# Kernel tuning notes

Hardware: AMD Instinct MI355X
Metric: run time of the kernel (lower is better)

Reference implementation:

```python
import jax, jax.numpy as jnp
import numpy as np

NF = 64   # num_feat
DG = 8    # deformable_groups (also conv groups)
B, H, W = 4, 96, 96
K = 9     # 3x3 kernel positions


def _conv(x, w, b, padding=1, dilation=1, groups=1):
    out = jax.lax.conv_general_dilated(
        x, w, (1, 1), [(padding, padding), (padding, padding)],
        rhs_dilation=(dilation, dilation),
        dimension_numbers=('NCHW', 'OIHW', 'NCHW'),
        feature_group_count=groups)
    return out + b[None, :, None, None]


def _lrelu(t):
    return jnp.where(t >= 0, t, 0.1 * t)


def _cat_align(a, b):
    # channel-interleaved concat: [a0,b0,a1,b1,...]
    Bn, k, h, w = a.shape
    return jnp.stack([a, b], axis=2).reshape(Bn, 2 * k, h, w)


def _deform_conv(x, offset, mask, weight, bias, dilation, padding):
    # DCNv2 modulated deformable conv, stride 1.
    Bn, C, h, w = x.shape
    Cpg = C // DG
    off = offset.reshape(Bn, DG, K, 2, h, w)          # (dy, dx) per group/kernel pos
    m = mask.reshape(Bn, DG, K, h, w)
    ky = (jnp.repeat(jnp.arange(3), 3) * dilation - padding).astype(x.dtype)  # (K,)
    kx = (jnp.tile(jnp.arange(3), 3) * dilation - padding).astype(x.dtype)
    hs = jnp.arange(h, dtype=x.dtype)
    ws = jnp.arange(w, dtype=x.dtype)
    py = off[:, :, :, 0] + ky[None, None, :, None, None] + hs[None, None, None, :, None]
    px = off[:, :, :, 1] + kx[None, None, :, None, None] + ws[None, None, None, None, :]
    y0f = jnp.floor(py); x0f = jnp.floor(px)
    ly = (py - y0f)[:, :, None]  # broadcast over Cpg
    lx = (px - x0f)[:, :, None]
    y0 = y0f.astype(jnp.int32); x0 = x0f.astype(jnp.int32)
    xg = x.reshape(Bn, DG, Cpg, h * w)

    def gather(yi, xi):
        inb = ((yi >= 0) & (yi < h) & (xi >= 0) & (xi < w))
        idx = (jnp.clip(yi, 0, h - 1) * w + jnp.clip(xi, 0, w - 1)).reshape(Bn, DG, 1, K * h * w)
        v = jnp.take_along_axis(xg, jnp.broadcast_to(idx, (Bn, DG, Cpg, K * h * w)), axis=3)
        return v.reshape(Bn, DG, Cpg, K, h, w) * inb[:, :, None].astype(x.dtype)

    v00 = gather(y0, x0); v01 = gather(y0, x0 + 1)
    v10 = gather(y0 + 1, x0); v11 = gather(y0 + 1, x0 + 1)
    val = (v00 * (1 - ly) * (1 - lx) + v01 * (1 - ly) * lx
           + v10 * ly * (1 - lx) + v11 * ly * lx) * m[:, :, None]
    sampled = val.reshape(Bn, C, K, h, w)
    out = jnp.einsum('bckhw,ock->bohw', sampled, weight.reshape(weight.shape[0], C, K))
    return out + bias[None, :, None, None]


def _dcn(x, off_feat, om_w, om_b, w, b, dilation):
    pad = dilation  # int(3/2)*dilation
    out = _conv(off_feat, om_w, om_b, padding=pad, dilation=dilation)
    o1, o2, msk = jnp.split(out, 3, axis=1)
    offset = jnp.concatenate([o1, o2], axis=1)
    mask = jax.nn.sigmoid(msk)
    return _deform_conv(x, offset, mask, w, b, dilation, pad)


def setup_inputs() -> dict:
    key = jax.random.key(0)
    ks = iter(jax.random.split(key, 64))
    def rn(shape, s=0.05):
        return jax.random.normal(next(ks), shape, jnp.float32) * s
    d = {}
    d['nbr_feat'] = jax.random.normal(next(ks), (B, NF, H, W), jnp.float32)
    d['ref_feat'] = jax.random.normal(next(ks), (B, NF, H, W), jnp.float32)
    for lv, has3 in [('l3', False), ('l2', True), ('l1', True)]:
        d[f'oc1_w_{lv}'] = rn((NF, 2 * NF // DG, 3, 3)); d[f'oc1_b_{lv}'] = rn((NF,))
        oc2_in = 2 * NF if has3 else NF
        d[f'oc2_w_{lv}'] = rn((NF, oc2_in // DG, 3, 3)); d[f'oc2_b_{lv}'] = rn((NF,))
        if has3:
            d[f'oc3_w_{lv}'] = rn((NF, NF // DG, 3, 3)); d[f'oc3_b_{lv}'] = rn((NF,))
            d[f'fc_w_{lv}'] = rn((NF, 2 * NF // DG, 3, 3)); d[f'fc_b_{lv}'] = rn((NF,))
        d[f'om_w_{lv}'] = rn((DG * 3 * K, NF, 3, 3), 0.01); d[f'om_b_{lv}'] = rn((DG * 3 * K,), 0.01)
        d[f'dcn_w_{lv}'] = rn((NF, NF, 3, 3)); d[f'dcn_b_{lv}'] = rn((NF,))
    d['cas_oc1_w'] = rn((NF, 2 * NF // DG, 3, 3)); d['cas_oc1_b'] = rn((NF,))
    d['cas_oc2_w'] = rn((NF, NF // DG, 3, 3)); d['cas_oc2_b'] = rn((NF,))
    d['cas_om_w'] = rn((DG * 3 * K, NF, 3, 3), 0.01); d['cas_om_b'] = rn((DG * 3 * K,), 0.01)
    d['cas_w'] = rn((NF, NF, 3, 3)); d['cas_b'] = rn((NF,))
    return d


def reference(nbr_feat, ref_feat,
              oc1_w_l3, oc1_b_l3, oc2_w_l3, oc2_b_l3, om_w_l3, om_b_l3, dcn_w_l3, dcn_b_l3,
              oc1_w_l2, oc1_b_l2, oc2_w_l2, oc2_b_l2, oc3_w_l2, oc3_b_l2, fc_w_l2, fc_b_l2,
              om_w_l2, om_b_l2, dcn_w_l2, dcn_b_l2,
              oc1_w_l1, oc1_b_l1, oc2_w_l1, oc2_b_l1, oc3_w_l1, oc3_b_l1, fc_w_l1, fc_b_l1,
              om_w_l1, om_b_l1, dcn_w_l1, dcn_b_l1,
              cas_oc1_w, cas_oc1_b, cas_oc2_w, cas_oc2_b, cas_om_w, cas_om_b, cas_w, cas_b):
    # level 3 (dilation 5)
    off = _lrelu(_conv(_cat_align(nbr_feat, ref_feat), oc1_w_l3, oc1_b_l3, groups=DG))
    off = _lrelu(_conv(off, oc2_w_l3, oc2_b_l3, groups=DG))
    feat = _lrelu(_dcn(nbr_feat, off, om_w_l3, om_b_l3, dcn_w_l3, dcn_b_l3, 5))
    to, tf = off, feat
    # level 2 (dilation 3)
    off = _lrelu(_conv(_cat_align(nbr_feat, ref_feat), oc1_w_l2, oc1_b_l2, groups=DG))
    off = _lrelu(_conv(_cat_align(off, to), oc2_w_l2, oc2_b_l2, groups=DG))
    off = _lrelu(_conv(off, oc3_w_l2, oc3_b_l2, groups=DG))
    feat = _dcn(nbr_feat, off, om_w_l2, om_b_l2, dcn_w_l2, dcn_b_l2, 3)
    feat = _lrelu(_conv(_cat_align(feat, tf), fc_w_l2, fc_b_l2, groups=DG))
    to, tf = off, feat
    # level 1 (dilation 1), no lrelu on feat
    off = _lrelu(_conv(_cat_align(nbr_feat, ref_feat), oc1_w_l1, oc1_b_l1, groups=DG))
    off = _lrelu(_conv(_cat_align(off, to), oc2_w_l1, oc2_b_l1, groups=DG))
    off = _lrelu(_conv(off, oc3_w_l1, oc3_b_l1, groups=DG))
    feat = _dcn(nbr_feat, off, om_w_l1, om_b_l1, dcn_w_l1, dcn_b_l1, 1)
    feat = _conv(_cat_align(feat, tf), fc_w_l1, fc_b_l1, groups=DG)
    # cascade
    off = _cat_align(feat, ref_feat)
    off = _lrelu(_conv(_lrelu(_conv(off, cas_oc1_w, cas_oc1_b, groups=DG)), cas_oc2_w, cas_oc2_b, groups=DG))
    feat = _lrelu(_dcn(feat, off, cas_om_w, cas_om_b, cas_w, cas_b, 1))
    return feat
```

## Files before the change

### kernel.cpp

```cpp
#include <hip/hip_runtime.h>

#define BATCH 4
#define NFEAT 64
#define DGRP 8
#define HH 96
#define WW 96
#define HWP (HH*WW)

typedef short short4a __attribute__((ext_vector_type(4)));
typedef short short8 __attribute__((ext_vector_type(8)));
typedef float f32x4 __attribute__((ext_vector_type(4)));
typedef float f32x16 __attribute__((ext_vector_type(16)));

__device__ inline short f2bf(float f) {
  union { float f; unsigned u; } v; v.f = f;
  unsigned r = v.u + 0x7fff + ((v.u >> 16) & 1);
  return (short)(r >> 16);
}
__device__ inline float bf2f(short s) {
  return __uint_as_float(((unsigned)(unsigned short)s) << 16);
}

__device__ __forceinline__ void barrier_keep_vmcnt() {
  asm volatile("s_waitcnt lgkmcnt(0)" ::: "memory");
  __builtin_amdgcn_s_barrier();
  asm volatile("" ::: "memory");
}

__global__ __launch_bounds__(256) void prep_om(
    const float* __restrict__ s0, const float* __restrict__ s1,
    const float* __restrict__ s2, const float* __restrict__ s3,
    short* __restrict__ dst) {
  int gid = blockIdx.x * 256 + threadIdx.x;
  if (gid >= 4 * 147456) return;
  int t = gid / 147456, r = gid % 147456;
  int tile = r / 18432, r2 = r % 18432;
  int kk = r2 / 512, r3 = r2 % 512;
  int lane = r3 / 8, j = r3 % 8;
  int col = lane & 31, half = lane >> 5;
  int oc = tile * 32 + col;
  int k = kk * 16 + half * 8 + j;
  int p = k >> 6, c = k & 63;
  const float* s = (t == 0) ? s0 : (t == 1) ? s1 : (t == 2) ? s2 : s3;
  float v = (oc < 216) ? s[(size_t)oc * 576 + c * 9 + p] : 0.f;
  dst[gid] = f2bf(v);
}

__global__ __launch_bounds__(256) void prep_dcnw(
    const float* __restrict__ s0, const float* __restrict__ s1,
    const float* __restrict__ s2, const float* __restrict__ s3,
    short* __restrict__ dst) {
  int gid = blockIdx.x * 256 + threadIdx.x;
  if (gid >= 4 * 36864) return;
  int t = gid / 36864, r = gid % 36864;
  int tile = r / 18432, r2 = r % 18432;
  int kk = r2 / 512, r3 = r2 % 512;
  int lane = r3 / 8, j = r3 % 8;
  int col = lane & 31, half = lane >> 5;
  int oc = tile * 32 + col;
  int k = kk * 16 + half * 8 + j;
  int p = k >> 6, c = k & 63;
  const float* s = (t == 0) ? s0 : (t == 1) ? s1 : (t == 2) ? s2 : s3;
  dst[gid] = f2bf(s[(size_t)oc * 576 + c * 9 + p]);
}

struct GwArgs {
  const float* src[12];
  int cat[12];
  int base[13];
};

__global__ __launch_bounds__(256) void prep_gw(GwArgs a, short* __restrict__ dst) {
  int gid = blockIdx.x * 256 + threadIdx.x;
  if (gid >= a.base[12]) return;
  int t = 0;
  while (gid >= a.base[t + 1]) ++t;
  int r = gid - a.base[t];
  const float* s = a.src[t];
  const int tsz = a.cat[t] ? 4608 : 2560;
  int tile = r / tsz, r2 = r % tsz;
  int kk = r2 / 512, r3 = r2 % 512;
  int lane = r3 >> 3, j = r3 & 7;
  int m = lane & 15, quad = lane >> 4;
  int oc = tile * 16 + m;
  int j32 = quad * 8 + j;
  float val = 0.f;
  if (a.cat[t]) {
    int gsel = j32 >> 4, ssel = (j32 >> 3) & 1, ch8 = j32 & 7;
    if (gsel == (m >> 3)) val = s[oc * 144 + (2 * ch8 + ssel) * 9 + kk];
  } else {
    int tapsel = j32 >> 4, gsel = (j32 >> 3) & 1, ch8 = j32 & 7;
    int p = 2 * kk + tapsel;
    if (p < 9 && gsel == (m >> 3)) val = s[oc * 72 + ch8 * 9 + p];
  }
  dst[gid] = f2bf(val);
}

__global__ __launch_bounds__(256) void transpose_bf16(
    const float* __restrict__ in0, short* __restrict__ out0,
    const float* __restrict__ in1, short* __restrict__ out1) {
  const float* in = blockIdx.z ? in1 : in0;
  short* out = blockIdx.z ? out1 : out0;
  __shared__ float s[64][65];
  const int p0 = blockIdx.x * 64;
  const int b = blockIdx.y;
  const int tx = threadIdx.x, ty = threadIdx.y;
  for (int c = ty; c < 64; c += 4)
    s[c][tx] = in[((size_t)b * NFEAT + c) * HWP + p0 + tx];
  __syncthreads();
  for (int p = ty; p < 64; p += 4)
    out[((size_t)b * HWP + p0 + p) * NFEAT + tx] = f2bf(s[tx][p]);
}

template <bool CAT, bool LRELU>
__device__ __forceinline__ void gconv_body(
    const short* __restrict__ in0, const short* __restrict__ in1,
    const short* __restrict__ Wsh, const float* __restrict__ bias,
    short* __restrict__ out, int pixbase, int b, int lid) {
  const int lane = lid & 63, t = lid >> 6;
  const int n = lane & 15, quad = lane >> 4;
  constexpr int NKK = CAT ? 9 : 5;

  short8 A[NKK];
#pragma unroll
  for (int kk = 0; kk < NKK; ++kk)
    A[kk] = *(const short8*)(Wsh + ((size_t)(t * NKK + kk) * 64 + lane) * 8);

  const short* sb;
  if (CAT) {
    sb = ((quad & 1) ? in1 : in0) + (size_t)b * HWP * 64 + (2 * t + (quad >> 1)) * 8;
  } else {
    sb = in0 + (size_t)b * HWP * 64 + (2 * t + (quad & 1)) * 8;
  }

  f32x4 acc[2] = {};
#pragma unroll
  for (int nt = 0; nt < 2; ++nt) {
    const int pix = pixbase + nt * 16 + n;
    const int yp = pix / WW, xp = pix % WW;
#pragma unroll
    for (int kk = 0; kk < NKK; ++kk) {
      const int p = CAT ? kk : (2 * kk + (quad >> 1));
      short8 B = {0, 0, 0, 0, 0, 0, 0, 0};
      if (p < 9) {
        const int sy = yp + p / 3 - 1, sx = xp + p % 3 - 1;
        if (((unsigned)sy < (unsigned)HH) && ((unsigned)sx < (unsigned)WW))
          B = *(const short8*)(sb + (size_t)(sy * WW + sx) * 64);
      }
      acc[nt] = __builtin_amdgcn_mfma_f32_16x16x32_bf16(A[kk], B, acc[nt], 0, 0, 0);
    }
  }

  const int ocb = t * 16 + quad * 4;
  const float b0 = bias[ocb], b1 = bias[ocb + 1], b2 = bias[ocb + 2], b3 = bias[ocb + 3];
#pragma unroll
  for (int nt = 0; nt < 2; ++nt) {
    float v0 = acc[nt][0] + b0, v1 = acc[nt][1] + b1;
    float v2 = acc[nt][2] + b2, v3 = acc[nt][3] + b3;
    if (LRELU) {
      v0 = (v0 >= 0.f) ? v0 : 0.1f * v0;
      v1 = (v1 >= 0.f) ? v1 : 0.1f * v1;
      v2 = (v2 >= 0.f) ? v2 : 0.1f * v2;
      v3 = (v3 >= 0.f) ? v3 : 0.1f * v3;
    }
    short4a pk = {f2bf(v0), f2bf(v1), f2bf(v2), f2bf(v3)};
    *(short4a*)(out + ((size_t)b * HWP + pixbase + nt * 16 + n) * 64 + ocb) = pk;
  }
}

template <bool CAT, bool LRELU>
__global__ __launch_bounds__(256) void gconv_mfma(
    const short* __restrict__ in0, const short* __restrict__ in1,
    const short* __restrict__ Wsh, const float* __restrict__ bias,
    short* __restrict__ out) {
  gconv_body<CAT, LRELU>(in0, in1, Wsh, bias, out, blockIdx.x * 32, blockIdx.y,
                         threadIdx.x);
}

struct Oc1Args {
  const short* W[3];
  const float* bias[3];
  short* out[3];
};

__global__ __launch_bounds__(256) void gconv_oc1x3(
    const short* __restrict__ in0, const short* __restrict__ in1, Oc1Args a) {
  const int job = blockIdx.z;
  gconv_body<true, true>(in0, in1, a.W[job], a.bias[job], a.out[job],
                         blockIdx.x * 32, blockIdx.y, threadIdx.x);
}

#define BPITCH 324
template <int D>
__device__ __forceinline__ void omconv_body(
    short* Bs,
    const short* __restrict__ pixT, const short* __restrict__ Wsh,
    const float* __restrict__ bias, short* __restrict__ out,
    int xblk, int b, int lid) {
  const int lane = lid & 63;
  const int w = lid >> 6;
  const int col = lane & 31, half = lane >> 5;
  const int pixbase = xblk * 64;

  const short* aP0 = Wsh + ((size_t)(w * 36) * 64) * 8 + (size_t)lane * 8;
  const short* aP1 = Wsh + ((size_t)((w + 4) * 36) * 64) * 8 + (size_t)lane * 8;
  const short* pixb = pixT + (size_t)b * HWP * 64;

  f32x16 acc00 = {}, acc01 = {}, acc10 = {}, acc11 = {};

  for (int i = lid; i < 64 * 5 * 8; i += 256) {
    int row = i / 40, q = i % 40;
    int p = q >> 3, c8 = q & 7;
    int pix = pixbase + row;
    int yp = pix / WW, xp = pix % WW;
    int sy = yp + (p / 3 - 1) * D, sx = xp + (p % 3 - 1) * D;
    short4a lo = {0, 0, 0, 0}, hi = {0, 0, 0, 0};
    if (((unsigned)sy < (unsigned)HH) && ((unsigned)sx < (unsigned)WW)) {
      const short* src = pixb + (size_t)(sy * WW + sx) * 64 + c8 * 8;
      lo = *(const short4a*)src;
      hi = *(const short4a*)(src + 4);
    }
    short* dst = Bs + row * BPITCH + q * 8;
    *(short4a*)dst = lo;
    *(short4a*)(dst + 4) = hi;
  }

  short4a p1lo[8], p1hi[8];
  int p1dst[8];
#pragma unroll
  for (int idx = 0; idx < 8; ++idx) {
    int i = lid + idx * 256;
    int row = i / 32, q = i % 32;
    int p = 5 + (q >> 3), c8 = q & 7;
    int pix = pixbase + row;
    int yp = pix / WW, xp = pix % WW;
    int sy = yp + (p / 3 - 1) * D, sx = xp + (p % 3 - 1) * D;
    short4a lo = {0, 0, 0, 0}, hi = {0, 0, 0, 0};
    if (((unsigned)sy < (unsigned)HH) && ((unsigned)sx < (unsigned)WW)) {
      const short* src = pixb + (size_t)(sy * WW + sx) * 64 + c8 * 8;
      lo = *(const short4a*)src;
      hi = *(const short4a*)(src + 4);
    }
    p1lo[idx] = lo;
    p1hi[idx] = hi;
    p1dst[idx] = row * BPITCH + q * 8;
  }
  barrier_keep_vmcnt();

#pragma unroll 4
  for (int kk = 0; kk < 20; ++kk) {
    short8 A0 = *(const short8*)(aP0 + (size_t)kk * 512);
    short8 A1 = *(const short8*)(aP1 + (size_t)kk * 512);
    const short* b0 = Bs + col * BPITCH + kk * 16 + half * 8;
    const short* b1 = Bs + (32 + col) * BPITCH + kk * 16 + half * 8;
    short4a l0 = *(const short4a*)b0, h0 = *(const short4a*)(b0 + 4);
    short4a l1 = *(const short4a*)b1, h1 = *(const short4a*)(b1 + 4);
    short8 B0 = {l0[0], l0[1], l0[2], l0[3], h0[0], h0[1], h0[2], h0[3]};
    short8 B1 = {l1[0], l1[1], l1[2], l1[3], h1[0], h1[1], h1[2], h1[3]};
    acc00 = __builtin_amdgcn_mfma_f32_32x32x16_bf16(A0, B0, acc00, 0, 0, 0);
    acc01 = __builtin_amdgcn_mfma_f32_32x32x16_bf16(A0, B1, acc01, 0, 0, 0);
    acc10 = __builtin_amdgcn_mfma_f32_32x32x16_bf16(A1, B0, acc10, 0, 0, 0);
    acc11 = __builtin_amdgcn_mfma_f32_32x32x16_bf16(A1, B1, acc11, 0, 0, 0);
  }
  barrier_keep_vmcnt();

#pragma unroll
  for (int idx = 0; idx < 8; ++idx) {
    short* dst = Bs + p1dst[idx];
    *(short4a*)dst = p1lo[idx];
    *(short4a*)(dst + 4) = p1hi[idx];
  }
  barrier_keep_vmcnt();

#pragma unroll 4
  for (int kk = 0; kk < 16; ++kk) {
    const int kkg = 20 + kk;
    short8 A0 = *(const short8*)(aP0 + (size_t)kkg * 512);
    short8 A1 = *(const short8*)(aP1 + (size_t)kkg * 512);
    const short* b0 = Bs + col * BPITCH + kk * 16 + half * 8;
    const short* b1 = Bs + (32 + col) * BPITCH + kk * 16 + half * 8;
    short4a l0 = *(const short4a*)b0, h0 = *(const short4a*)(b0 + 4);
    short4a l1 = *(const short4a*)b1, h1 = *(const short4a*)(b1 + 4);
    short8 B0 = {l0[0], l0[1], l0[2], l0[3], h0[0], h0[1], h0[2], h0[3]};
    short8 B1 = {l1[0], l1[1], l1[2], l1[3], h1[0], h1[1], h1[2], h1[3]};
    acc00 = __builtin_amdgcn_mfma_f32_32x32x16_bf16(A0, B0, acc00, 0, 0, 0);
    acc01 = __builtin_amdgcn_mfma_f32_32x32x16_bf16(A0, B1, acc01, 0, 0, 0);
    acc10 = __builtin_amdgcn_mfma_f32_32x32x16_bf16(A1, B0, acc10, 0, 0, 0);
    acc11 = __builtin_amdgcn_mfma_f32_32x32x16_bf16(A1, B1, acc11, 0, 0, 0);
  }

  const int pix0 = pixbase + col, pix1 = pixbase + 32 + col;
#pragma unroll
  for (int r = 0; r < 16; ++r) {
    const int rrow = (r & 3) + 8 * (r >> 2) + 4 * half;
    const int oc0 = w * 32 + rrow;
    const int oc1 = (w + 4) * 32 + rrow;
    const float bs0 = bias[oc0];
    out[((size_t)b * 216 + oc0) * HWP + pix0] = f2bf(acc00[r] + bs0);
    out[((size_t)b * 216 + oc0) * HWP + pix1] = f2bf(acc01[r] + bs0);
    if (oc1 < 216) {
      const float bs1 = bias[oc1];
      out[((size_t)b * 216 + oc1) * HWP + pix0] = f2bf(acc10[r] + bs1);
      out[((size_t)b * 216 + oc1) * HWP + pix1] = f2bf(acc11[r] + bs1);
    }
  }
}

template <int D>
__global__ __launch_bounds__(256) void omconv_mfma(
    const short* __restrict__ pixT, const short* __restrict__ Wsh,
    const float* __restrict__ bias, short* __restrict__ out) {
  __shared__ short Bs[64 * BPITCH];
  omconv_body<D>(Bs, pixT, Wsh, bias, out, blockIdx.x, blockIdx.y, threadIdx.x);
}

template <int D, bool LRELU, bool PMOUT>
__device__ __forceinline__ void dcn_body(
    char* smem,
    const short* __restrict__ xT, const short* __restrict__ om,
    const short* __restrict__ Wd, const float* __restrict__ bias,
    void* __restrict__ outv, int pb, int b, int lid) {
  short* Ls = (short*)smem;
  float* red = (float*)(smem + 36864);
  const int tx = lid & 31, ty = lid >> 5;

  {
    const int px = tx, dg = ty;
    const int pix = pb * 32 + px;
    const int yp = pix / WW, xp = pix % WW;
    const size_t bOM = (size_t)b * 216 * HWP;
    const short* xb = xT + (size_t)b * HWP * 64 + dg * 8;
    short* Sp = Ls + (size_t)((dg & 1) * 32 + px) * 8;

#pragma unroll
    for (int k = 0; k < 9; ++k) {
      float dy = bf2f(om[bOM + (size_t)(dg * 18 + 2 * k) * HWP + pix]);
      float dxv = bf2f(om[bOM + (size_t)(dg * 18 + 2 * k + 1) * HWP + pix]);
      float mr = bf2f(om[bOM + (size_t)(144 + dg * 9 + k) * HWP + pix]);
      float m = 1.f / (1.f + __expf(-mr));
      float py = (float)(yp + (k / 3 - 1) * D) + dy;
      float px_ = (float)(xp + (k % 3 - 1) * D) + dxv;
      float y0f = floorf(py), x0f = floorf(px_);
      float ly = py - y0f, lx = px_ - x0f;
      int y0 = (int)y0f, x0 = (int)x0f;
      int y1 = y0 + 1, x1 = x0 + 1;
      bool vy0 = (unsigned)y0 < (unsigned)HH, vy1 = (unsigned)y1 < (unsigned)HH;
      bool vx0 = (unsigned)x0 < (unsigned)WW, vx1 = (unsigned)x1 < (unsigned)WW;
      int cy0 = min(max(y0, 0), HH - 1), cy1 = min(max(y1, 0), HH - 1);
      int cx0 = min(max(x0, 0), WW - 1), cx1 = min(max(x1, 0), WW - 1);
      float w00 = (vy0 && vx0) ? (1.f - ly) * (1.f - lx) * m : 0.f;
      float w01 = (vy0 && vx1) ? (1.f - ly) * lx * m : 0.f;
      float w10 = (vy1 && vx0) ? ly * (1.f - lx) * m : 0.f;
      float w11 = (vy1 && vx1) ? ly * lx * m : 0.f;
      short8 s00 = *(const short8*)(xb + (size_t)(cy0 * WW + cx0) * 64);
      short8 s01 = *(const short8*)(xb + (size_t)(cy0 * WW + cx1) * 64);
      short8 s10 = *(const short8*)(xb + (size_t)(cy1 * WW + cx0) * 64);
      short8 s11 = *(const short8*)(xb + (size_t)(cy1 * WW + cx1) * 64);
      short8 pk;
#pragma unroll
      for (int cl = 0; cl < 8; ++cl) {
        float v = w00 * bf2f(s00[cl]) + w01 * bf2f(s01[cl]) +
                  w10 * bf2f(s10[cl]) + w11 * bf2f(s11[cl]);
        pk[cl] = f2bf(v);
      }
      const int kk = k * 4 + (dg >> 1);
      *(short8*)(Sp + (size_t)kk * 512) = pk;
    }
  }
  __syncthreads();

  const int lane = lid & 63, w = lid >> 6;
  const int col = lane & 31, half = lane >> 5;
  const int octile = w & 1, kh = w >> 1;
  const int pix = pb * 32 + col;

  const short* aP = Wd + ((size_t)(octile * 36) * 64 + lane) * 8;
  const short* bP = Ls + (size_t)lane * 8;

  f32x16 acc = {};
#pragma unroll 6
  for (int kk = 0; kk < 18; ++kk) {
    const int kkg = kh * 18 + kk;
    short8 A = *(const short8*)(aP + (size_t)kkg * 512);
    short8 B = *(const short8*)(bP + (size_t)kkg * 512);
    acc = __builtin_amdgcn_mfma_f32_32x32x16_bf16(A, B, acc, 0, 0, 0);
  }

  if (kh == 1) {
#pragma unroll
    for (int r = 0; r < 16; ++r) red[((size_t)octile * 64 + lane) * 17 + r] = acc[r];
  }
  __syncthreads();
  if (kh == 0) {
    const float* rp = red + ((size_t)octile * 64 + lane) * 17;
    if (PMOUT) {
      short* out = (short*)outv;
#pragma unroll
      for (int rg = 0; rg < 4; ++rg) {
        short4a pk;
#pragma unroll
        for (int i = 0; i < 4; ++i) {
          const int r = rg * 4 + i;
          const int oc = octile * 32 + i + 8 * rg + 4 * half;
          float v = acc[r] + rp[r] + bias[oc];
          if (LRELU) v = (v >= 0.f) ? v : 0.1f * v;
          pk[i] = f2bf(v);
        }
        *(short4a*)(out + ((size_t)b * HWP + pix) * 64 + octile * 32 + 8 * rg + 4 * half) = pk;
      }
    } else {
      float* out = (float*)outv;
#pragma unroll
      for (int r = 0; r < 16; ++r) {
        const int oc = octile * 32 + (r & 3) + 8 * (r >> 2) + 4 * half;
        float v = acc[r] + rp[r] + bias[oc];
        if (LRELU) v = (v >= 0.f) ? v : 0.1f * v;
        out[((size_t)b * NFEAT + oc) * HWP + pix] = v;
      }
    }
  }
}

template <int D, bool LRELU, bool PMOUT>
__global__ __launch_bounds__(256) void dcn_fused(
    const short* __restrict__ xT, const short* __restrict__ om,
    const short* __restrict__ Wd, const float* __restrict__ bias,
    void* __restrict__ outv) {
  __shared__ char smem[45568];
  dcn_body<D, LRELU, PMOUT>(smem, xT, om, Wd, bias, outv,
                            blockIdx.x, blockIdx.y, threadIdx.x);
}

template <int D>
__global__ __launch_bounds__(256) void om_gc(
    const short* __restrict__ pixT, const short* __restrict__ Wom,
    const float* __restrict__ obias, short* __restrict__ omOut,
    const short* __restrict__ g0, const short* __restrict__ g1,
    const short* __restrict__ gW, const float* __restrict__ gb,
    short* __restrict__ gout) {
  __shared__ short Bs[64 * BPITCH];
  if (blockIdx.x < 144)
    omconv_body<D>(Bs, pixT, Wom, obias, omOut, blockIdx.x, blockIdx.y, threadIdx.x);
  else
    gconv_body<true, true>(g0, g1, gW, gb, gout, (blockIdx.x - 144) * 32,
                           blockIdx.y, threadIdx.x);
}

template <int D, bool DLRELU>
__global__ __launch_bounds__(256) void dcn_gc(
    const short* __restrict__ xT, const short* __restrict__ om,
    const short* __restrict__ Wd, const float* __restrict__ dbias,
    short* __restrict__ dout,
    const short* __restrict__ g0, const short* __restrict__ gW,
    const float* __restrict__ gb, short* __restrict__ gout) {
  __shared__ char smem[45568];
  if (blockIdx.x < 288)
    dcn_body<D, DLRELU, true>(smem, xT, om, Wd, dbias, dout,
                              blockIdx.x, blockIdx.y, threadIdx.x);
  else
    gconv_body<false, true>(g0, nullptr, gW, gb, gout, (blockIdx.x - 288) * 32,
                            blockIdx.y, threadIdx.x);
}

extern "C" void kernel_launch(void* const* d_in, const int* in_sizes, int n_in,
                              void* d_out, int out_size, void* d_ws, size_t ws_size,
                              hipStream_t stream) {
  const float* nbr = (const float*)d_in[0];
  const float* ref = (const float*)d_in[1];
  auto f = [&](int i) { return (const float*)d_in[i]; };

  short* s0 = (short*)d_ws;
  const size_t PM = (size_t)BATCH * HWP * 64;
  short* omB = s0;
  short* refT = omB + 7962624;
  short* pmA = refT + PM;
  short* pmB = pmA + PM;
  short* pmC = pmB + PM;
  short* pmD = pmC + PM;
  short* pmE = pmD + PM;
  short* pmF = pmE + PM;
  short* pmG = pmF + PM;
  short* wbf = pmG + PM;
  short* wdcn = wbf + 589824;
  short* wgc = wdcn + 147456;
  short* nbrT = (short*)d_out;

  prep_om<<<(4 * 147456 + 255) / 256, 256, 0, stream>>>(f(6), f(18), f(30), f(38), wbf);
  prep_dcnw<<<(4 * 36864 + 255) / 256, 256, 0, stream>>>(f(8), f(20), f(32), f(40), wdcn);

  static const int gSrc[12] = {2, 4, 10, 12, 14, 16, 22, 24, 26, 28, 34, 36};
  static const int gCat[12] = {1, 0, 1, 1, 0, 1, 1, 1, 0, 1, 1, 0};
  GwArgs ga;
  int gb = 0;
  const short* wg[12];
  for (int t = 0; t < 12; ++t) {
    ga.src[t] = f(gSrc[t]);
    ga.cat[t] = gCat[t];
    ga.base[t] = gb;
    wg[t] = wgc + gb;
    gb += gCat[t] ? 18432 : 10240;
  }
  ga.base[12] = gb;
  prep_gw<<<(gb + 255) / 256, 256, 0, stream>>>(ga, wgc);

  short* wbf_l3 = wbf;
  short* wbf_l2 = wbf + 147456;
  short* wbf_l1 = wbf + 2 * 147456;
  short* wbf_cas = wbf + 3 * 147456;
  short* wd_l3 = wdcn;
  short* wd_l2 = wdcn + 36864;
  short* wd_l1 = wdcn + 2 * 36864;
  short* wd_cas = wdcn + 3 * 36864;

  dim3 gcGrid(288, BATCH);
  dim3 oc1Grid(288, BATCH, 3);
  dim3 omgcGrid(432, BATCH);
  dim3 dcngcGrid(576, BATCH);
  dim3 omGrid(144, BATCH);
  dim3 dfGrid(288, BATCH);
  dim3 trGrid(HWP / 64, BATCH, 2), trBlk(64, 4);

  transpose_bf16<<<trGrid, trBlk, 0, stream>>>(nbr, nbrT, ref, refT);

  Oc1Args oa;
  oa.W[0] = wg[0]; oa.bias[0] = f(3);  oa.out[0] = pmA;
  oa.W[1] = wg[2]; oa.bias[1] = f(11); oa.out[1] = pmF;
  oa.W[2] = wg[6]; oa.bias[2] = f(23); oa.out[2] = pmG;
  gconv_oc1x3<<<oc1Grid, 256, 0, stream>>>(nbrT, refT, oa);

  gconv_mfma<false, true><<<gcGrid, 256, 0, stream>>>(pmA, nullptr, wg[1], f(5), pmB);

  om_gc<5><<<omgcGrid, 256, 0, stream>>>(pmB, wbf_l3, f(7), omB,
                                         pmF, pmB, wg[3], f(13), pmD);
  dcn_gc<5, true><<<dcngcGrid, 256, 0, stream>>>(nbrT, omB, wd_l3, f(9), pmC,
                                                 pmD, wg[4], f(15), pmE);
  om_gc<3><<<omgcGrid, 256, 0, stream>>>(pmE, wbf_l2, f(19), omB,
                                         pmG, pmE, wg[7], f(25), pmB);
  dcn_gc<3, false><<<dcngcGrid, 256, 0, stream>>>(nbrT, omB, wd_l2, f(21), pmD,
                                                  pmB, wg[8], f(27), pmF);
  om_gc<1><<<omgcGrid, 256, 0, stream>>>(pmF, wbf_l1, f(31), omB,
                                         pmD, pmC, wg[5], f(17), pmA);
  dcn_fused<1, false, true><<<dfGrid, 256, 0, stream>>>(nbrT, omB, wd_l1, f(33), pmE);
  gconv_mfma<true, false><<<gcGrid, 256, 0, stream>>>(pmE, pmA, wg[9], f(29), pmB);

  gconv_mfma<true, true><<<gcGrid, 256, 0, stream>>>(pmB, refT, wg[10], f(35), pmC);
  gconv_mfma<false, true><<<gcGrid, 256, 0, stream>>>(pmC, nullptr, wg[11], f(37), pmD);
  omconv_mfma<1><<<omGrid, 256, 0, stream>>>(pmD, wbf_cas, f(39), omB);
  dcn_fused<1, true, false><<<dfGrid, 256, 0, stream>>>(pmB, omB, wd_cas, f(41), (float*)d_out);
}
```

Measured before the change: 505.3 us.

## Fuse prep kernels, halve omconv pixel tile, and alias DCN reduction smem

Merges the four preprocessing launches (input transposes plus three weight-reformat kernels) into a single fused kernel to cut launch overhead and serialization. Halves the omconv tile from 64 to 32 pixels per block, which doubles its grid and halves its LDS footprint and accumulator registers. The DCN reduction buffer now aliases the sample tile, with an added barrier, shrinking shared memory. Together these aim for higher occupancy and better SM fill, at the cost of reloading weights for each smaller tile.

```diff
diff --git a/kernel.cpp b/kernel.cpp
--- a/kernel.cpp
+++ b/kernel.cpp
@@ -27,12 +27,14 @@
   asm volatile("" ::: "memory");
 }
 
-__global__ __launch_bounds__(256) void prep_om(
-    const float* __restrict__ s0, const float* __restrict__ s1,
-    const float* __restrict__ s2, const float* __restrict__ s3,
-    short* __restrict__ dst) {
-  int gid = blockIdx.x * 256 + threadIdx.x;
-  if (gid >= 4 * 147456) return;
+struct GwArgs {
+  const float* src[12];
+  int cat[12];
+  int base[13];
+};
+
+__device__ __forceinline__ void prep_om_elem(
+    int gid, const float* const* s4, short* __restrict__ dst) {
   int t = gid / 147456, r = gid % 147456;
   int tile = r / 18432, r2 = r % 18432;
   int kk = r2 / 512, r3 = r2 % 512;
@@ -41,17 +43,12 @@
   int oc = tile * 32 + col;
   int k = kk * 16 + half * 8 + j;
   int p = k >> 6, c = k & 63;
-  const float* s = (t == 0) ? s0 : (t == 1) ? s1 : (t == 2) ? s2 : s3;
-  float v = (oc < 216) ? s[(size_t)oc * 576 + c * 9 + p] : 0.f;
+  float v = (oc < 216) ? s4[t][(size_t)oc * 576 + c * 9 + p] : 0.f;
   dst[gid] = f2bf(v);
 }
 
-__global__ __launch_bounds__(256) void prep_dcnw(
-    const float* __restrict__ s0, const float* __restrict__ s1,
-    const float* __restrict__ s2, const float* __restrict__ s3,
-    short* __restrict__ dst) {
-  int gid = blockIdx.x * 256 + threadIdx.x;
-  if (gid >= 4 * 36864) return;
+__device__ __forceinline__ void prep_dcnw_elem(
+    int gid, const float* const* s4, short* __restrict__ dst) {
   int t = gid / 36864, r = gid % 36864;
   int tile = r / 18432, r2 = r % 18432;
   int kk = r2 / 512, r3 = r2 % 512;
@@ -60,19 +57,11 @@
   int oc = tile * 32 + col;
   int k = kk * 16 + half * 8 + j;
   int p = k >> 6, c = k & 63;
-  const float* s = (t == 0) ? s0 : (t == 1) ? s1 : (t == 2) ? s2 : s3;
-  dst[gid] = f2bf(s[(size_t)oc * 576 + c * 9 + p]);
-}
-
-struct GwArgs {
-  const float* src[12];
-  int cat[12];
-  int base[13];
-};
-
-__global__ __launch_bounds__(256) void prep_gw(GwArgs a, short* __restrict__ dst) {
-  int gid = blockIdx.x * 256 + threadIdx.x;
-  if (gid >= a.base[12]) return;
+  dst[gid] = f2bf(s4[t][(size_t)oc * 576 + c * 9 + p]);
+}
+
+__device__ __forceinline__ void prep_gw_elem(
+    int gid, const GwArgs& a, short* __restrict__ dst) {
   int t = 0;
   while (gid >= a.base[t + 1]) ++t;
   int r = gid - a.base[t];
@@ -96,20 +85,35 @@
   dst[gid] = f2bf(val);
 }
 
-__global__ __launch_bounds__(256) void transpose_bf16(
-    const float* __restrict__ in0, short* __restrict__ out0,
-    const float* __restrict__ in1, short* __restrict__ out1) {
-  const float* in = blockIdx.z ? in1 : in0;
-  short* out = blockIdx.z ? out1 : out0;
+struct PrepArgs {
+  const float* nbr; const float* ref;
+  short* nbrT; short* refT;
+  const float* omS[4]; short* wbf;
+  const float* dwS[4]; short* wdcn;
+  GwArgs gw; short* wgc;
+};
+
+__global__ __launch_bounds__(256) void prep_fused(PrepArgs a) {
   __shared__ float s[64][65];
-  const int p0 = blockIdx.x * 64;
-  const int b = blockIdx.y;
-  const int tx = threadIdx.x, ty = threadIdx.y;
-  for (int c = ty; c < 64; c += 4)
-    s[c][tx] = in[((size_t)b * NFEAT + c) * HWP + p0 + tx];
-  __syncthreads();
-  for (int p = ty; p < 64; p += 4)
-    out[((size_t)b * HWP + p0 + p) * NFEAT + tx] = f2bf(s[tx][p]);
+  const int bx = blockIdx.x;
+  const int lid = threadIdx.x;
+  if (bx < 1152) {
+    const int x = bx % 144, b = (bx / 144) & 3, z = bx / 576;
+    const float* in = z ? a.ref : a.nbr;
+    short* out = z ? a.refT : a.nbrT;
+    const int p0 = x * 64;
+    const int tx = lid & 63, ty = lid >> 6;
+    for (int c = ty; c < 64; c += 4)
+      s[c][tx] = in[((size_t)b * NFEAT + c) * HWP + p0 + tx];
+    __syncthreads();
+    for (int p = ty; p < 64; p += 4)
+      out[((size_t)b * HWP + p0 + p) * NFEAT + tx] = f2bf(s[tx][p]);
+  } else {
+    const int gid = (bx - 1152) * 256 + lid;
+    if (gid < 589824) prep_om_elem(gid, a.omS, a.wbf);
+    else if (gid < 737280) prep_dcnw_elem(gid - 589824, a.dwS, a.wdcn);
+    else if (gid < 925696) prep_gw_elem(gid - 737280, a.gw, a.wgc);
+  }
 }
 
 template <bool CAT, bool LRELU>
@@ -200,15 +204,15 @@
   const int lane = lid & 63;
   const int w = lid >> 6;
   const int col = lane & 31, half = lane >> 5;
-  const int pixbase = xblk * 64;
+  const int pixbase = xblk * 32;
 
   const short* aP0 = Wsh + ((size_t)(w * 36) * 64) * 8 + (size_t)lane * 8;
   const short* aP1 = Wsh + ((size_t)((w + 4) * 36) * 64) * 8 + (size_t)lane * 8;
   const short* pixb = pixT + (size_t)b * HWP * 64;
 
-  f32x16 acc00 = {}, acc01 = {}, acc10 = {}, acc11 = {};
-
-  for (int i = lid; i < 64 * 5 * 8; i += 256) {
+  f32x16 acc00 = {}, acc10 = {};
+
+  for (int i = lid; i < 32 * 5 * 8; i += 256) {
     int row = i / 40, q = i % 40;
     int p = q >> 3, c8 = q & 7;
     int pix = pixbase + row;
@@ -225,10 +229,10 @@
     *(short4a*)(dst + 4) = hi;
   }
 
-  short4a p1lo[8], p1hi[8];
-  int p1dst[8];
-#pragma unroll
-  for (int idx = 0; idx < 8; ++idx) {
+  short4a p1lo[4], p1hi[4];
+  int p1dst[4];
+#pragma unroll
+  for (int idx = 0; idx < 4; ++idx) {
     int i = lid + idx * 256;
     int row = i / 32, q = i % 32;
     int p = 5 + (q >> 3), c8 = q & 7;
@@ -252,20 +256,15 @@
     short8 A0 = *(const short8*)(aP0 + (size_t)kk * 512);
     short8 A1 = *(const short8*)(aP1 + (size_t)kk * 512);
     const short* b0 = Bs + col * BPITCH + kk * 16 + half * 8;
-    const short* b1 = Bs + (32 + col) * BPITCH + kk * 16 + half * 8;
     short4a l0 = *(const short4a*)b0, h0 = *(const short4a*)(b0 + 4);
-    short4a l1 = *(const short4a*)b1, h1 = *(const short4a*)(b1 + 4);
     short8 B0 = {l0[0], l0[1], l0[2], l0[3], h0[0], h0[1], h0[2], h0[3]};
-    short8 B1 = {l1[0], l1[1], l1[2], l1[3], h1[0], h1[1], h1[2], h1[3]};
     acc00 = __builtin_amdgcn_mfma_f32_32x32x16_bf16(A0, B0, acc00, 0, 0, 0);
-    acc01 = __builtin_amdgcn_mfma_f32_32x32x16_bf16(A0, B1, acc01, 0, 0, 0);
     acc10 = __builtin_amdgcn_mfma_f32_32x32x16_bf16(A1, B0, acc10, 0, 0, 0);
-    acc11 = __builtin_amdgcn_mfma_f32_32x32x16_bf16(A1, B1, acc11, 0, 0, 0);
   }
   barrier_keep_vmcnt();
 
 #pragma unroll
-  for (int idx = 0; idx < 8; ++idx) {
+  for (int idx = 0; idx < 4; ++idx) {
     short* dst = Bs + p1dst[idx];
     *(short4a*)dst = p1lo[idx];
     *(short4a*)(dst + 4) = p1hi[idx];
@@ -278,31 +277,21 @@
     short8 A0 = *(const short8*)(aP0 + (size_t)kkg * 512);
     short8 A1 = *(const short8*)(aP1 + (size_t)kkg * 512);
     const short* b0 = Bs + col * BPITCH + kk * 16 + half * 8;
-    const short* b1 = Bs + (32 + col) * BPITCH + kk * 16 + half * 8;
     short4a l0 = *(const short4a*)b0, h0 = *(const short4a*)(b0 + 4);
-    short4a l1 = *(const short4a*)b1, h1 = *(const short4a*)(b1 + 4);
     short8 B0 = {l0[0], l0[1], l0[2], l0[3], h0[0], h0[1], h0[2], h0[3]};
-    short8 B1 = {l1[0], l1[1], l1[2], l1[3], h1[0], h1[1], h1[2], h1[3]};
     acc00 = __builtin_amdgcn_mfma_f32_32x32x16_bf16(A0, B0, acc00, 0, 0, 0);
-    acc01 = __builtin_amdgcn_mfma_f32_32x32x16_bf16(A0, B1, acc01, 0, 0, 0);
     acc10 = __builtin_amdgcn_mfma_f32_32x32x16_bf16(A1, B0, acc10, 0, 0, 0);
-    acc11 = __builtin_amdgcn_mfma_f32_32x32x16_bf16(A1, B1, acc11, 0, 0, 0);
-  }
-
-  const int pix0 = pixbase + col, pix1 = pixbase + 32 + col;
+  }
+
+  const int pix0 = pixbase + col;
 #pragma unroll
   for (int r = 0; r < 16; ++r) {
     const int rrow = (r & 3) + 8 * (r >> 2) + 4 * half;
     const int oc0 = w * 32 + rrow;
     const int oc1 = (w + 4) * 32 + rrow;
-    const float bs0 = bias[oc0];
-    out[((size_t)b * 216 + oc0) * HWP + pix0] = f2bf(acc00[r] + bs0);
-    out[((size_t)b * 216 + oc0) * HWP + pix1] = f2bf(acc01[r] + bs0);
-    if (oc1 < 216) {
-      const float bs1 = bias[oc1];
-      out[((size_t)b * 216 + oc1) * HWP + pix0] = f2bf(acc10[r] + bs1);
-      out[((size_t)b * 216 + oc1) * HWP + pix1] = f2bf(acc11[r] + bs1);
-    }
+    out[((size_t)b * 216 + oc0) * HWP + pix0] = f2bf(acc00[r] + bias[oc0]);
+    if (oc1 < 216)
+      out[((size_t)b * 216 + oc1) * HWP + pix0] = f2bf(acc10[r] + bias[oc1]);
   }
 }
 
@@ -310,7 +299,7 @@
 __global__ __launch_bounds__(256) void omconv_mfma(
     const short* __restrict__ pixT, const short* __restrict__ Wsh,
     const float* __restrict__ bias, short* __restrict__ out) {
-  __shared__ short Bs[64 * BPITCH];
+  __shared__ short Bs[32 * BPITCH];
   omconv_body<D>(Bs, pixT, Wsh, bias, out, blockIdx.x, blockIdx.y, threadIdx.x);
 }
 
@@ -321,7 +310,7 @@
     const short* __restrict__ Wd, const float* __restrict__ bias,
     void* __restrict__ outv, int pb, int b, int lid) {
   short* Ls = (short*)smem;
-  float* red = (float*)(smem + 36864);
+  float* red = (float*)smem;
   const int tx = lid & 31, ty = lid >> 5;
 
   {
@@ -385,6 +374,7 @@
     short8 B = *(const short8*)(bP + (size_t)kkg * 512);
     acc = __builtin_amdgcn_mfma_f32_32x32x16_bf16(A, B, acc, 0, 0, 0);
   }
+  __syncthreads();
 
   if (kh == 1) {
 #pragma unroll
@@ -426,7 +416,7 @@
     const short* __restrict__ xT, const short* __restrict__ om,
     const short* __restrict__ Wd, const float* __restrict__ bias,
     void* __restrict__ outv) {
-  __shared__ char smem[45568];
+  __shared__ __align__(16) char smem[36864];
   dcn_body<D, LRELU, PMOUT>(smem, xT, om, Wd, bias, outv,
                             blockIdx.x, blockIdx.y, threadIdx.x);
 }
@@ -438,11 +428,11 @@
     const short* __restrict__ g0, const short* __restrict__ g1,
     const short* __restrict__ gW, const float* __restrict__ gb,
     short* __restrict__ gout) {
-  __shared__ short Bs[64 * BPITCH];
-  if (blockIdx.x < 144)
+  __shared__ short Bs[32 * BPITCH];
+  if (blockIdx.x < 288)
     omconv_body<D>(Bs, pixT, Wom, obias, omOut, blockIdx.x, blockIdx.y, threadIdx.x);
   else
-    gconv_body<true, true>(g0, g1, gW, gb, gout, (blockIdx.x - 144) * 32,
+    gconv_body<true, true>(g0, g1, gW, gb, gout, (blockIdx.x - 288) * 32,
                            blockIdx.y, threadIdx.x);
 }
 
@@ -453,7 +443,7 @@
     short* __restrict__ dout,
     const short* __restrict__ g0, const short* __restrict__ gW,
     const float* __restrict__ gb, short* __restrict__ gout) {
-  __shared__ char smem[45568];
+  __shared__ __align__(16) char smem[36864];
   if (blockIdx.x < 288)
     dcn_body<D, DLRELU, true>(smem, xT, om, Wd, dbias, dout,
                               blockIdx.x, blockIdx.y, threadIdx.x);
@@ -485,9 +475,6 @@
   short* wgc = wdcn + 147456;
   short* nbrT = (short*)d_out;
 
-  prep_om<<<(4 * 147456 + 255) / 256, 256, 0, stream>>>(f(6), f(18), f(30), f(38), wbf);
-  prep_dcnw<<<(4 * 36864 + 255) / 256, 256, 0, stream>>>(f(8), f(20), f(32), f(40), wdcn);
-
   static const int gSrc[12] = {2, 4, 10, 12, 14, 16, 22, 24, 26, 28, 34, 36};
   static const int gCat[12] = {1, 0, 1, 1, 0, 1, 1, 1, 0, 1, 1, 0};
   GwArgs ga;
@@ -501,7 +488,15 @@
     gb += gCat[t] ? 18432 : 10240;
   }
   ga.base[12] = gb;
-  prep_gw<<<(gb + 255) / 256, 256, 0, stream>>>(ga, wgc);
+
+  PrepArgs pa;
+  pa.nbr = nbr; pa.ref = ref; pa.nbrT = nbrT; pa.refT = refT;
+  pa.omS[0] = f(6);  pa.omS[1] = f(18); pa.omS[2] = f(30); pa.omS[3] = f(38);
+  pa.wbf = wbf;
+  pa.dwS[0] = f(8);  pa.dwS[1] = f(20); pa.dwS[2] = f(32); pa.dwS[3] = f(40);
+  pa.wdcn = wdcn;
+  pa.gw = ga; pa.wgc = wgc;
+  prep_fused<<<dim3(4768), 256, 0, stream>>>(pa);
 
   short* wbf_l3 = wbf;
   short* wbf_l2 = wbf + 147456;
@@ -514,13 +509,10 @@
 
   dim3 gcGrid(288, BATCH);
   dim3 oc1Grid(288, BATCH, 3);
-  dim3 omgcGrid(432, BATCH);
+  dim3 omgcGrid(576, BATCH);
   dim3 dcngcGrid(576, BATCH);
-  dim3 omGrid(144, BATCH);
+  dim3 omGrid(288, BATCH);
   dim3 dfGrid(288, BATCH);
-  dim3 trGrid(HWP / 64, BATCH, 2), trBlk(64, 4);
-
-  transpose_bf16<<<trGrid, trBlk, 0, stream>>>(nbr, nbrT, ref, refT);
 
   Oc1Args oa;
   oa.W[0] = wg[0]; oa.bias[0] = f(3);  oa.out[0] = pmA;
```

Measured after the change: 507.3 us (median of 2 runs). Within noise of the previous version (+0.4%).
